# Optimization experiments

Hardware: AMD Instinct MI355X
Metric: run time of the kernel (lower is better)

The kernel has to match this reference:

```python
import jax, jax.numpy as jnp
import numpy as np

N_NODES = 100000
N_EDGES = 1000000
IN_F = 64
HID = 64
N_GRAPHS = 1000
HEADS = 4
NOTES = 128
NUM_MPNNS = 4
NUM_CONVS = 2
NUM_LINEARS = 3  # num_hidden_layers=2 -> 3 Linear layers in GIN MLP
EPS_BN = 1e-5


def setup_inputs() -> dict:
    key = jax.random.key(0)
    ks = jax.random.split(key, 16)
    s = 0.05
    x = jax.random.normal(ks[0], (N_NODES, IN_F), dtype=jnp.float32)
    edge_index = jax.random.randint(ks[1], (2, N_EDGES), 0, N_NODES)
    batch = jnp.sort(jax.random.randint(ks[2], (N_NODES,), 0, N_GRAPHS))
    dh = HID // HEADS
    return {
        'x': x,
        'edge_index': edge_index,
        'batch': batch,
        # feature BatchNorm affine params
        'fn_gamma': jnp.ones((IN_F,), jnp.float32),
        'fn_beta': jnp.zeros((IN_F,), jnp.float32),
        # input projection
        'proj_W': jax.random.normal(ks[3], (IN_F, HID), jnp.float32) * s,
        'proj_b': jnp.zeros((HID,), jnp.float32),
        # GIN MLPs: [num_mpnns, num_linears, HID, HID]
        'mlp_W': jax.random.normal(ks[4], (NUM_MPNNS, NUM_LINEARS, HID, HID), jnp.float32) * s,
        'mlp_b': jnp.zeros((NUM_MPNNS, NUM_LINEARS, HID), jnp.float32),
        # per-block conv BatchNorm affine params
        'norm_gamma': jnp.ones((NUM_MPNNS, HID), jnp.float32),
        'norm_beta': jnp.zeros((NUM_MPNNS, HID), jnp.float32),
        # attention readout (PMA-style): learned seed query per head
        'attn_seed': jax.random.normal(ks[5], (HEADS, dh), jnp.float32) * s,
        'attn_Wk': jax.random.normal(ks[6], (HID, HID), jnp.float32) * s,
        'attn_Wv': jax.random.normal(ks[7], (HID, HID), jnp.float32) * s,
        'attn_Wo': jax.random.normal(ks[8], (HID, HID), jnp.float32) * s,
        # notes predictor
        'pred_W': jax.random.normal(ks[9], (HID, NOTES), jnp.float32) * s,
        'pred_b': jnp.zeros((NOTES,), jnp.float32),
    }


def _batchnorm(z, gamma, beta):
    # training-mode BatchNorm1d over the node dimension (biased variance)
    mu = jnp.mean(z, axis=0)
    var = jnp.var(z, axis=0)
    return (z - mu) * jax.lax.rsqrt(var + EPS_BN) * gamma + beta


def reference(x, edge_index, batch, fn_gamma, fn_beta, proj_W, proj_b,
              mlp_W, mlp_b, norm_gamma, norm_beta,
              attn_seed, attn_Wk, attn_Wv, attn_Wo, pred_W, pred_b):
    src, dst = edge_index[0], edge_index[1]

    # feature norm + projection (dropout = identity at inference)
    h = _batchnorm(x, fn_gamma, fn_beta)
    h = jax.nn.relu(h @ proj_W + proj_b)
    residual = h

    # GINConv blocks: h' = MLP((1+eps)*h + sum_{j in N(i)} h_j), eps=0
    for m in range(NUM_MPNNS):
        for _ in range(NUM_CONVS):
            agg = h + jax.ops.segment_sum(h[src], dst, num_segments=N_NODES)
            z = agg
            for l in range(NUM_LINEARS):
                z = z @ mlp_W[m, l] + mlp_b[m, l]
                if l < NUM_LINEARS - 1:
                    z = jax.nn.relu(z)
            z = _batchnorm(z, norm_gamma[m], norm_beta[m])
            h = jax.nn.relu(z)
        h = h + residual
        residual = h

    # attention readout (PMA-style set attention pooling per graph)
    dh = HID // HEADS
    k = (h @ attn_Wk).reshape(N_NODES, HEADS, dh)
    v = (h @ attn_Wv).reshape(N_NODES, HEADS, dh)
    scores = jnp.einsum('nhd,hd->nh', k, attn_seed) / jnp.sqrt(jnp.float32(dh))
    smax = jax.ops.segment_max(scores, batch, num_segments=N_GRAPHS)  # [G,H]
    e = jnp.exp(scores - smax[batch])
    denom = jax.ops.segment_sum(e, batch, num_segments=N_GRAPHS)  # [G,H]
    attn = e / denom[batch]  # [N,H]
    pooled = jax.ops.segment_sum(attn[:, :, None] * v, batch, num_segments=N_GRAPHS)  # [G,H,dh]
    embed = pooled.reshape(N_GRAPHS, HID) @ attn_Wo  # [G, HID]

    logits = embed @ pred_W + pred_b
    return embed, logits
```

## Files before the change

kernel.cpp:

```cpp
#include <hip/hip_runtime.h>

typedef __attribute__((ext_vector_type(8))) short bf16x8;
typedef __attribute__((ext_vector_type(4))) float floatx4;

__device__ __forceinline__ unsigned short f2bf(float f)
{
    union { float f; unsigned int u; } v; v.f = f;
    unsigned int r = (v.u + 0x7fffu + ((v.u >> 16) & 1u)) >> 16;
    return (unsigned short)r;
}
__device__ __forceinline__ float bf2f(unsigned short b)
{
    union { unsigned int u; float f; } v; v.u = ((unsigned int)b) << 16;
    return v.f;
}

#define MFMA3(accv, ah, al, bh, bl)                                              \
    accv = __builtin_amdgcn_mfma_f32_16x16x32_bf16(ah, bh, accv, 0, 0, 0);       \
    accv = __builtin_amdgcn_mfma_f32_16x16x32_bf16(al, bh, accv, 0, 0, 0);       \
    accv = __builtin_amdgcn_mfma_f32_16x16x32_bf16(ah, bl, accv, 0, 0, 0);

#define BFRAG(P, n, kc, qd) (*(const bf16x8*)((P) + ((n) << 6) + (kc) * 32 + (qd) * 8))

__device__ __forceinline__ void pack_pair(const float* f, bf16x8& hi, bf16x8& lo)
{
#pragma unroll
    for (int j = 0; j < 8; ++j) {
        unsigned short hb = f2bf(f[j]);
        hi[j] = (short)hb;
        lo[j] = (short)f2bf(f[j] - bf2f(hb));
    }
}

__device__ __forceinline__ floatx4 gxform(uint2 raw, floatx4 sc4, floatx4 sh4)
{
    floatx4 v;
    v[0] = bf2f((unsigned short)(raw.x & 0xffffu));
    v[1] = bf2f((unsigned short)(raw.x >> 16));
    v[2] = bf2f((unsigned short)(raw.y & 0xffffu));
    v[3] = bf2f((unsigned short)(raw.y >> 16));
    floatx4 r;
#pragma unroll
    for (int j = 0; j < 4; ++j) r[j] = fmaxf(fmaf(v[j], sc4[j], sh4[j]), 0.f);
    return r;
}


__global__ void k_prep(const float* __restrict__ pW, const float* __restrict__ mlpW,
                       const float* __restrict__ Wv,
                       short* __restrict__ preH, short* __restrict__ preL)
{
    int mat = blockIdx.x;
    const float* Wg = (mat == 0) ? pW : ((mat <= 12) ? mlpW + (size_t)(mat - 1) * 4096 : Wv);
    int t = threadIdx.x;
    short* dh = preH + (size_t)mat * 4096;
    short* dl = preL + (size_t)mat * 4096;
#pragma unroll
    for (int i = 0; i < 16; ++i) {
        int idx = i * 256 + t;
        int k = idx >> 6, n = idx & 63;
        float w = Wg[idx];
        unsigned short hb = f2bf(w);
        dh[n * 64 + k] = (short)hb;
        dl[n * 64 + k] = (short)f2bf(w - bf2f(hb));
    }
}


__global__ void k_count(const int* __restrict__ dst, int* __restrict__ cnt, int E)
{
    for (int e = blockIdx.x * 256 + threadIdx.x; e < E; e += gridDim.x * 256)
        atomicAdd(&cnt[dst[e]], 1);
}

__global__ void k_scan1(const int* __restrict__ cnt, int* __restrict__ bsum, int n)
{
    __shared__ int red[256];
    int t = threadIdx.x;
    int i = blockIdx.x * 256 + t;
    red[t] = (i < n) ? cnt[i] : 0;
    __syncthreads();
    for (int off = 128; off; off >>= 1) {
        if (t < off) red[t] += red[t + off];
        __syncthreads();
    }
    if (t == 0) bsum[blockIdx.x] = red[0];
}

__global__ void k_scan2(const int* __restrict__ bsum, int* __restrict__ boff,
                        int nb, int* __restrict__ rowptrN)
{
    __shared__ int sc[512];
    int t = threadIdx.x;
    int v = (t < nb) ? bsum[t] : 0;
    sc[t] = v;
    __syncthreads();
    for (int off = 1; off < 512; off <<= 1) {
        int u = (t >= off) ? sc[t - off] : 0;
        __syncthreads();
        sc[t] += u;
        __syncthreads();
    }
    if (t < nb) boff[t] = sc[t] - v;
    if (t == nb - 1) *rowptrN = sc[t];
}

__global__ void k_scan3(int* __restrict__ cnt, const int* __restrict__ boff,
                        int* __restrict__ rowptr, int n)
{
    __shared__ int sc[256];
    int t = threadIdx.x;
    int i = blockIdx.x * 256 + t;
    int v = (i < n) ? cnt[i] : 0;
    sc[t] = v;
    __syncthreads();
    for (int off = 1; off < 256; off <<= 1) {
        int u = (t >= off) ? sc[t - off] : 0;
        __syncthreads();
        sc[t] += u;
        __syncthreads();
    }
    if (i < n) {
        rowptr[i] = boff[blockIdx.x] + sc[t] - v;
        cnt[i] = 0;
    }
}

__global__ void k_fill(const int* __restrict__ src, const int* __restrict__ dst,
                       const int* __restrict__ rowptr, int* __restrict__ cursor,
                       int* __restrict__ col, int E)
{
    for (int e = blockIdx.x * 256 + threadIdx.x; e < E; e += gridDim.x * 256) {
        int d = dst[e];
        int p = atomicAdd(&cursor[d], 1);
        col[rowptr[d] + p] = src[e];
    }
}


__global__ void k_xstats(const float* __restrict__ x, float* __restrict__ stats, int N)
{
    __shared__ float rs[256], rq[256];
    int t = threadIdx.x;
    int f = t & 63, rg = t >> 6;
    float s = 0.f, q = 0.f;
    for (int r = blockIdx.x * 4 + rg; r < N; r += gridDim.x * 4) {
        float v = x[(size_t)r * 64 + f];
        s += v; q += v * v;
    }
    rs[rg * 64 + f] = s; rq[rg * 64 + f] = q;
    __syncthreads();
    if (t < 64) {
        float ts = rs[t] + rs[64 + t] + rs[128 + t] + rs[192 + t];
        float tq = rq[t] + rq[64 + t] + rq[128 + t] + rq[192 + t];
        int rep = (blockIdx.x & 3) * 128;
        atomicAdd(&stats[rep + t], ts);
        atomicAdd(&stats[rep + 64 + t], tq);
    }
}

__device__ __forceinline__ void finalize_lds(const float* __restrict__ stats,
                                             const float* __restrict__ gamma,
                                             const float* __restrict__ beta,
                                             float* __restrict__ SS, int t, float invN)
{
    if (t < 64) {
        float su = stats[t] + stats[128 + t] + stats[256 + t] + stats[384 + t];
        float qu = stats[64 + t] + stats[192 + t] + stats[320 + t] + stats[448 + t];
        float mu = su * invN;
        float var = qu * invN - mu * mu;
        float sc = gamma[t] * rsqrtf(var + 1e-5f);
        SS[t] = sc;
        SS[64 + t] = beta[t] - mu * sc;
    }
}


__global__ void __launch_bounds__(256, 4)
k_proj(const float* __restrict__ x, const float* __restrict__ stats,
       const float* __restrict__ fn_g, const float* __restrict__ fn_b,
       const short* __restrict__ WH, const short* __restrict__ WL,
       const float* __restrict__ b,
       unsigned short* __restrict__ hbh, unsigned short* __restrict__ hbl,
       int N, float invN)
{
    __shared__ float ScSh[128];
    __shared__ float BiasSh[64];
    int t = threadIdx.x;
    int wave = t >> 6, lane = t & 63;
    int m = lane & 15, qd = lane >> 4;
    int base = blockIdx.x * 64;
    int nodeA = base + wave * 16 + m;

    finalize_lds(stats, fn_g, fn_b, ScSh, t, invN);
    if (t < 64) BiasSh[t] = b[t];
    __syncthreads();

    int rowc = min(nodeA, N - 1);
    bf16x8 ah[2], al[2];
#pragma unroll
    for (int kc = 0; kc < 2; ++kc) {
        floatx4 x0 = *(const floatx4*)(x + (size_t)rowc * 64 + kc * 32 + qd * 8);
        floatx4 x1 = *(const floatx4*)(x + (size_t)rowc * 64 + kc * 32 + qd * 8 + 4);
        float av[8];
#pragma unroll
        for (int j = 0; j < 8; ++j) {
            int k = kc * 32 + qd * 8 + j;
            float xv = (j < 4) ? x0[j] : x1[j - 4];
            av[j] = xv * ScSh[k] + ScSh[64 + k];
        }
        pack_pair(av, ah[kc], al[kc]);
    }

    floatx4 acc[4];
#pragma unroll
    for (int tt = 0; tt < 4; ++tt) {
        float bv = BiasSh[tt * 16 + m];
        acc[tt] = (floatx4){bv, bv, bv, bv};
    }
#pragma unroll
    for (int kc = 0; kc < 2; ++kc)
#pragma unroll
        for (int tt = 0; tt < 4; ++tt) {
            bf16x8 bh = BFRAG(WH, tt * 16 + m, kc, qd);
            bf16x8 bl = BFRAG(WL, tt * 16 + m, kc, qd);
            MFMA3(acc[tt], ah[kc], al[kc], bh, bl);
        }

#pragma unroll
    for (int tt = 0; tt < 4; ++tt)
#pragma unroll
        for (int r = 0; r < 4; ++r) {
            int node = base + wave * 16 + qd * 4 + r;
            if (node < N) {
                int col = tt * 16 + m;
                float v = fmaxf(acc[tt][r], 0.f);
                size_t off = (size_t)node * 64 + col;
                unsigned short ph = f2bf(v);
                hbh[off] = ph;
                hbl[off] = f2bf(v - bf2f(ph));
            }
        }
}


__global__ void __launch_bounds__(256, 8)
k_conv(const unsigned short* __restrict__ gsrc,
       const int* __restrict__ rowptr, const int* __restrict__ col,
       const short* __restrict__ WH, const short* __restrict__ WL,
       const float* __restrict__ b3,
       const float* __restrict__ pstats, const float* __restrict__ gamma,
       const float* __restrict__ beta,
       float* __restrict__ zout, unsigned short* __restrict__ zbout,
       float* __restrict__ stats, int N, int mode, float invN)
{
    __shared__ __align__(16) float Aint[64 * 68];
    __shared__ float BiasSh[192];
    __shared__ __align__(16) float SS[128];
    int t = threadIdx.x;
    int wave = t >> 6, lane = t & 63;
    int m = lane & 15, qd = lane >> 4;
    int base = blockIdx.x * 64;
    float* Aw = Aint + wave * 1088;

    if (t < 192) BiasSh[t] = b3[t];
    if (mode) {
        finalize_lds(pstats, gamma, beta, SS, t, invN);
    } else if (t < 128) {
        SS[t] = (t < 64) ? 1.f : 0.f;
    }
    __syncthreads();

    int g4 = lane >> 4;
    int fq = lane & 15;
    floatx4 sc4 = *(const floatx4*)(SS + 4 * fq);
    floatx4 sh4 = *(const floatx4*)(SS + 64 + 4 * fq);
    const unsigned short* gp = gsrc + fq * 4;

#pragma unroll 1
    for (int i = 0; i < 16; ++i) {
        int node = base + wave * 16 + i;
        floatx4 a4 = {0.f, 0.f, 0.f, 0.f};
        if (node < N) {
            {
                uint2 raw = *(const uint2*)(gp + (size_t)node * 64);
                floatx4 vv = gxform(raw, sc4, sh4);
                if (g4 == 0) a4 += vv;
            }
            int e0 = rowptr[node], e1 = rowptr[node + 1];
            int e = e0;
            for (; e + 8 <= e1; e += 8) {
                int s0 = col[e + g4], s1 = col[e + 4 + g4];
                uint2 r0 = *(const uint2*)(gp + (size_t)s0 * 64);
                uint2 r1 = *(const uint2*)(gp + (size_t)s1 * 64);
                a4 += gxform(r0, sc4, sh4);
                a4 += gxform(r1, sc4, sh4);
            }
            if (e + 4 <= e1) {
                int s0 = col[e + g4];
                uint2 r0 = *(const uint2*)(gp + (size_t)s0 * 64);
                a4 += gxform(r0, sc4, sh4);
                e += 4;
            }
            if (e < e1) {
                int ee = e + g4;
                int s0 = col[min(ee, e1 - 1)];
                uint2 r0 = *(const uint2*)(gp + (size_t)s0 * 64);
                floatx4 vv = gxform(r0, sc4, sh4);
                if (ee < e1) a4 += vv;
            }
#pragma unroll
            for (int j = 0; j < 4; ++j) {
                float v = a4[j];
                v += __shfl_xor(v, 16, 64);
                v += __shfl_xor(v, 32, 64);
                a4[j] = v;
            }
        }
        if (g4 == 0) *(floatx4*)(Aw + i * 68 + fq * 4) = a4;
    }
    __syncthreads();

    floatx4 acc[4];

#pragma unroll 1
    for (int l = 0; l < 3; ++l) {
        const short* LH = WH + l * 4096;
        const short* LL = WL + l * 4096;
#pragma unroll
        for (int tt = 0; tt < 4; ++tt) {
            float bv = BiasSh[l * 64 + tt * 16 + m];
            acc[tt] = (floatx4){bv, bv, bv, bv};
        }
#pragma unroll
        for (int kc = 0; kc < 2; ++kc) {
            floatx4 x0 = *(const floatx4*)(Aw + m * 68 + kc * 32 + qd * 8);
            floatx4 x1 = *(const floatx4*)(Aw + m * 68 + kc * 32 + qd * 8 + 4);
            float av[8];
#pragma unroll
            for (int j = 0; j < 8; ++j) av[j] = (j < 4) ? x0[j] : x1[j - 4];
            bf16x8 ah, al;
            pack_pair(av, ah, al);
#pragma unroll
            for (int tt = 0; tt < 4; ++tt) {
                bf16x8 bh = BFRAG(LH, tt * 16 + m, kc, qd);
                bf16x8 bl = BFRAG(LL, tt * 16 + m, kc, qd);
                MFMA3(acc[tt], ah, al, bh, bl);
            }
        }
        if (l < 2) {
            __syncthreads();
#pragma unroll
            for (int tt = 0; tt < 4; ++tt)
#pragma unroll
                for (int r = 0; r < 4; ++r)
                    Aw[(qd * 4 + r) * 68 + tt * 16 + m] = fmaxf(acc[tt][r], 0.f);
            __syncthreads();
        }
    }

#pragma unroll
    for (int tt = 0; tt < 4; ++tt)
#pragma unroll
        for (int r = 0; r < 4; ++r) {
            int node = base + wave * 16 + qd * 4 + r;
            if (node < N) {
                size_t off = (size_t)node * 64 + tt * 16 + m;
                if (mode) zout[off] = acc[tt][r];
                else      zbout[off] = f2bf(acc[tt][r]);
            }
        }

    __syncthreads();
    float* SW = Aint;
#pragma unroll
    for (int tt = 0; tt < 4; ++tt) {
        float s = 0.f, q = 0.f;
#pragma unroll
        for (int r = 0; r < 4; ++r) {
            int node = base + wave * 16 + qd * 4 + r;
            float v = (node < N) ? acc[tt][r] : 0.f;
            s += v; q += v * v;
        }
        SW[(tt * 16 + m) * 16 + wave * 4 + qd] = s;
        SW[2048 + (tt * 16 + m) * 16 + wave * 4 + qd] = q;
    }
    __syncthreads();
    if (t < 64) {
        float s = 0.f, q = 0.f;
#pragma unroll
        for (int i = 0; i < 16; ++i) { s += SW[t * 16 + i]; q += SW[2048 + t * 16 + i]; }
        int rep = (blockIdx.x & 3) * 128;
        atomicAdd(&stats[rep + t], s);
        atomicAdd(&stats[rep + 64 + t], q);
    }
}


__global__ void k_bnrelu(const float4* __restrict__ z4,
                         const float* __restrict__ stats, const float* __restrict__ gamma,
                         const float* __restrict__ beta,
                         ushort4* __restrict__ hbh4, ushort4* __restrict__ hbl4,
                         int total4, float invN)
{
    __shared__ float SS[128];
    int t = threadIdx.x;
    finalize_lds(stats, gamma, beta, SS, t, invN);
    __syncthreads();
    for (int idx = blockIdx.x * 256 + t; idx < total4; idx += gridDim.x * 256) {
        int c = (idx & 15) << 2;
        float4 v = z4[idx];
        ushort4 rh = hbh4[idx];
        ushort4 rl = hbl4[idx];
        v.x = fmaxf(v.x * SS[c + 0] + SS[64 + c + 0], 0.f) + (bf2f(rh.x) + bf2f(rl.x));
        v.y = fmaxf(v.y * SS[c + 1] + SS[64 + c + 1], 0.f) + (bf2f(rh.y) + bf2f(rl.y));
        v.z = fmaxf(v.z * SS[c + 2] + SS[64 + c + 2], 0.f) + (bf2f(rh.z) + bf2f(rl.z));
        v.w = fmaxf(v.w * SS[c + 3] + SS[64 + c + 3], 0.f) + (bf2f(rh.w) + bf2f(rl.w));
        ushort4 ph, pl;
        ph.x = f2bf(v.x); ph.y = f2bf(v.y); ph.z = f2bf(v.z); ph.w = f2bf(v.w);
        pl.x = f2bf(v.x - bf2f(ph.x));
        pl.y = f2bf(v.y - bf2f(ph.y));
        pl.z = f2bf(v.z - bf2f(ph.z));
        pl.w = f2bf(v.w - bf2f(ph.w));
        hbh4[idx] = ph;
        hbl4[idx] = pl;
    }
}


__global__ void __launch_bounds__(256, 4)
k_bnvs(const float* __restrict__ z,
       const unsigned short* __restrict__ hbh, const unsigned short* __restrict__ hbl,
       const float* __restrict__ stats, const float* __restrict__ gamma,
       const float* __restrict__ beta,
       const short* __restrict__ WH, const short* __restrict__ WL,
       const float* __restrict__ Wk, const float* __restrict__ seed,
       float* __restrict__ v, float* __restrict__ scores, int N, float invN)
{
    __shared__ float ScSh[128];
    __shared__ short Sh[16 * 72], Sl[16 * 72];
    int t = threadIdx.x;
    int wave = t >> 6, lane = t & 63;
    int m = lane & 15, qd = lane >> 4;
    int base = blockIdx.x * 64;
    int nodeA = base + wave * 16 + m;

    finalize_lds(stats, gamma, beta, ScSh, t, invN);
    {
        int k = t >> 2, n = t & 3;
        float s = 0.f;
#pragma unroll
        for (int d = 0; d < 16; ++d) s += Wk[k * 64 + n * 16 + d] * seed[n * 16 + d];
        s *= 0.25f;
        unsigned short hb = f2bf(s);
        Sh[n * 72 + k] = (short)hb;
        Sl[n * 72 + k] = (short)f2bf(s - bf2f(hb));
        unsigned int* Z1 = (unsigned int*)(Sh + 4 * 72);
        unsigned int* Z2 = (unsigned int*)(Sl + 4 * 72);
        for (int idx2 = t; idx2 < 432; idx2 += 256) { Z1[idx2] = 0; Z2[idx2] = 0; }
    }
    __syncthreads();

    int rowc = min(nodeA, N - 1);
    bf16x8 ah[2], al[2];
#pragma unroll
    for (int kc = 0; kc < 2; ++kc) {
        floatx4 z0 = *(const floatx4*)(z + (size_t)rowc * 64 + kc * 32 + qd * 8);
        floatx4 z1 = *(const floatx4*)(z + (size_t)rowc * 64 + kc * 32 + qd * 8 + 4);
        bf16x8 rh = *(const bf16x8*)(hbh + (size_t)rowc * 64 + kc * 32 + qd * 8);
        bf16x8 rl = *(const bf16x8*)(hbl + (size_t)rowc * 64 + kc * 32 + qd * 8);
        float av[8];
#pragma unroll
        for (int j = 0; j < 8; ++j) {
            int k = kc * 32 + qd * 8 + j;
            float zv = (j < 4) ? z0[j] : z1[j - 4];
            float rv = bf2f((unsigned short)rh[j]) + bf2f((unsigned short)rl[j]);
            av[j] = fmaxf(zv * ScSh[k] + ScSh[64 + k], 0.f) + rv;
        }
        pack_pair(av, ah[kc], al[kc]);
    }

    floatx4 acc[5] = {};
#pragma unroll
    for (int kc = 0; kc < 2; ++kc) {
#pragma unroll
        for (int tt = 0; tt < 4; ++tt) {
            bf16x8 bh = BFRAG(WH, tt * 16 + m, kc, qd);
            bf16x8 bl = BFRAG(WL, tt * 16 + m, kc, qd);
            MFMA3(acc[tt], ah[kc], al[kc], bh, bl);
        }
        bf16x8 sh = *(const bf16x8*)(Sh + m * 72 + kc * 32 + qd * 8);
        bf16x8 sl = *(const bf16x8*)(Sl + m * 72 + kc * 32 + qd * 8);
        MFMA3(acc[4], ah[kc], al[kc], sh, sl);
    }

#pragma unroll
    for (int tt = 0; tt < 4; ++tt)
#pragma unroll
        for (int r = 0; r < 4; ++r) {
            int node = base + wave * 16 + qd * 4 + r;
            if (node < N)
                v[(size_t)node * 64 + tt * 16 + m] = acc[tt][r];
        }
    if (m < 4) {
#pragma unroll
        for (int r = 0; r < 4; ++r) {
            int node = base + wave * 16 + qd * 4 + r;
            if (node < N) scores[(size_t)node * 4 + m] = acc[4][r];
        }
    }
}


__global__ void k_tail(const float4* __restrict__ scores4, const float* __restrict__ v,
                       const int* __restrict__ batch,
                       const float* __restrict__ Wo, const float* __restrict__ predW,
                       const float* __restrict__ predb,
                       float* __restrict__ emb, float* __restrict__ logits, int N)
{
    int g = blockIdx.x;
    int t = threadIdx.x;
    __shared__ int sb[2];
    __shared__ float4 rmax[256];
    __shared__ float racc[256];
    __shared__ float resum[16];
    __shared__ float pooledSh[64];
    __shared__ float embSh[64];
    if (t < 2) {
        int target = g + t;
        int lo = 0, hi = N;
        while (lo < hi) {
            int mid = (lo + hi) >> 1;
            if (batch[mid] < target) lo = mid + 1; else hi = mid;
        }
        sb[t] = lo;
    }
    __syncthreads();
    int s = sb[0], e = sb[1];
    if (s >= e) {
        if (t < 64) pooledSh[t] = 0.f;
    } else {
        float4 m = make_float4(-1e30f, -1e30f, -1e30f, -1e30f);
        for (int i = s + t; i < e; i += 256) {
            float4 sc = scores4[i];
            m.x = fmaxf(m.x, sc.x); m.y = fmaxf(m.y, sc.y);
            m.z = fmaxf(m.z, sc.z); m.w = fmaxf(m.w, sc.w);
        }
        rmax[t] = m;
        __syncthreads();
        for (int off = 128; off; off >>= 1) {
            if (t < off) {
                float4 a = rmax[t], b = rmax[t + off];
                a.x = fmaxf(a.x, b.x); a.y = fmaxf(a.y, b.y);
                a.z = fmaxf(a.z, b.z); a.w = fmaxf(a.w, b.w);
                rmax[t] = a;
            }
            __syncthreads();
        }
        float4 smax = rmax[0];
        int rg = t >> 6, f = t & 63, hh = f >> 4;
        float mx = (hh == 0) ? smax.x : ((hh == 1) ? smax.y : ((hh == 2) ? smax.z : smax.w));
        float acc = 0.f, es = 0.f;
        for (int i = s + rg; i < e; i += 4) {
            float4 sc = scores4[i];
            float scl = (hh == 0) ? sc.x : ((hh == 1) ? sc.y : ((hh == 2) ? sc.z : sc.w));
            float ev = __expf(scl - mx);
            acc += ev * v[(size_t)i * 64 + f];
            if ((f & 15) == 0) es += ev;
        }
        racc[rg * 64 + f] = acc;
        if ((f & 15) == 0) resum[rg * 4 + hh] = es;
        __syncthreads();
        if (t < 64) {
            float tot = racc[t] + racc[64 + t] + racc[128 + t] + racc[192 + t];
            int h2 = t >> 4;
            float den = resum[h2] + resum[4 + h2] + resum[8 + h2] + resum[12 + h2];
            pooledSh[t] = tot / den;
        }
    }
    __syncthreads();

    if (t < 64) {
        float s2 = 0.f;
#pragma unroll 4
        for (int k = 0; k < 64; ++k) s2 = fmaf(pooledSh[k], Wo[k * 64 + t], s2);
        embSh[t] = s2;
        emb[(size_t)g * 64 + t] = s2;
    }
    __syncthreads();

    if (t < 128) {
        float s2 = predb[t];
#pragma unroll 4
        for (int k = 0; k < 64; ++k) s2 = fmaf(embSh[k], predW[k * 128 + t], s2);
        logits[(size_t)g * 128 + t] = s2;
    }
}


extern "C" void kernel_launch(void* const* d_in, const int* in_sizes, int n_in,
                              void* d_out, int out_size, void* d_ws, size_t ws_size,
                              hipStream_t stream)
{
    const float* x     = (const float*)d_in[0];
    const int*   eidx  = (const int*)d_in[1];
    const int*   batch = (const int*)d_in[2];
    const float* fn_g  = (const float*)d_in[3];
    const float* fn_b  = (const float*)d_in[4];
    const float* pW    = (const float*)d_in[5];
    const float* pb    = (const float*)d_in[6];
    const float* mlpW  = (const float*)d_in[7];
    const float* mlpb  = (const float*)d_in[8];
    const float* ngm   = (const float*)d_in[9];
    const float* nbt   = (const float*)d_in[10];
    const float* seed  = (const float*)d_in[11];
    const float* Wk    = (const float*)d_in[12];
    const float* Wv    = (const float*)d_in[13];
    const float* Wo    = (const float*)d_in[14];
    const float* predW = (const float*)d_in[15];
    const float* predb = (const float*)d_in[16];

    const int N = 100000, E = 1000000, G = 1000;
    const int* srcv = eidx;
    const int* dstv = eidx + E;

    char* w = (char*)d_ws;
    auto alloc = [&](size_t bytes) {
        char* p = w;
        w += (bytes + 255) & ~(size_t)255;
        return p;
    };
    const size_t NPAD = 100032;
    float*          z    = (float*)alloc(NPAD * 64 * 4);
    unsigned short* hbh  = (unsigned short*)alloc(NPAD * 64 * 2);
    unsigned short* hbl  = (unsigned short*)alloc(NPAD * 64 * 2);
    unsigned short* zb   = (unsigned short*)alloc(NPAD * 64 * 2);
    short* preH = (short*)alloc(14 * 4096 * 2);
    short* preL = (short*)alloc(14 * 4096 * 2);
    int*   rowptr = (int*)alloc((size_t)(N + 1) * 4);
    int*   cnt    = (int*)alloc((size_t)N * 4);
    int*   col    = (int*)alloc((size_t)E * 4);
    int*   bsum   = (int*)alloc(512 * 4);
    int*   boff   = (int*)alloc(512 * 4);
    float* stats  = (float*)alloc(9 * 512 * 4);
    float* scores = (float*)alloc(NPAD * 4 * 4);

    float* emb    = (float*)d_out;
    float* logits = (float*)d_out + G * 64;

    const int NB = (N + 63) / 64;
    const int NBS = (N + 255) / 256;
    const float invN = 1.f / (float)N;

    hipMemsetAsync(cnt, 0, (size_t)N * 4, stream);
    hipMemsetAsync(stats, 0, 9 * 512 * 4, stream);
    k_prep<<<14, 256, 0, stream>>>(pW, mlpW, Wv, preH, preL);
    k_count<<<1024, 256, 0, stream>>>(dstv, cnt, E);
    k_scan1<<<NBS, 256, 0, stream>>>(cnt, bsum, N);
    k_scan2<<<1, 512, 0, stream>>>(bsum, boff, NBS, rowptr + N);
    k_scan3<<<NBS, 256, 0, stream>>>(cnt, boff, rowptr, N);
    k_fill<<<1024, 256, 0, stream>>>(srcv, dstv, rowptr, cnt, col, E);

    k_xstats<<<512, 256, 0, stream>>>(x, stats, N);
    k_proj<<<NB, 256, 0, stream>>>(x, stats, fn_g, fn_b, preH, preL, pb, hbh, hbl, N, invN);

    for (int m = 0; m < 4; ++m) {
        int mat = 1 + m * 3;
        const short* WH = preH + (size_t)mat * 4096;
        const short* WL = preL + (size_t)mat * 4096;
        const float* b3 = mlpb + (size_t)m * 3 * 64;
        float* st0 = stats + (size_t)(1 + m * 2) * 512;
        float* st1 = stats + (size_t)(2 + m * 2) * 512;

        k_conv<<<NB, 256, 0, stream>>>(hbh, rowptr, col, WH, WL, b3,
                                       nullptr, nullptr, nullptr,
                                       nullptr, zb, st0, N, 0, invN);
        k_conv<<<NB, 256, 0, stream>>>(zb, rowptr, col, WH, WL, b3,
                                       st0, ngm + m * 64, nbt + m * 64,
                                       z, nullptr, st1, N, 1, invN);
        if (m < 3)
            k_bnrelu<<<2048, 256, 0, stream>>>(
                (const float4*)z, st1, ngm + m * 64, nbt + m * 64,
                (ushort4*)hbh, (ushort4*)hbl, N * 16, invN);
    }

    float* vbuf = z;
    k_bnvs<<<NB, 256, 0, stream>>>(z, hbh, hbl, stats + 8 * 512, ngm + 192, nbt + 192,
                                   preH + 13 * 4096, preL + 13 * 4096,
                                   Wk, seed, vbuf, scores, N, invN);
    k_tail<<<G, 256, 0, stream>>>((const float4*)scores, vbuf, batch,
                                  Wo, predW, predb, emb, logits, N);
}
```

Baseline: 955.6 us.

## Merge setup kernels: fold memsets into prep, co-launch count/xstats and fill/proj

```diff
diff --git a/kernel.cpp b/kernel.cpp
--- a/kernel.cpp
+++ b/kernel.cpp
@@ -48,103 +48,46 @@
 
 __global__ void k_prep(const float* __restrict__ pW, const float* __restrict__ mlpW,
                        const float* __restrict__ Wv,
-                       short* __restrict__ preH, short* __restrict__ preL)
-{
-    int mat = blockIdx.x;
-    const float* Wg = (mat == 0) ? pW : ((mat <= 12) ? mlpW + (size_t)(mat - 1) * 4096 : Wv);
-    int t = threadIdx.x;
-    short* dh = preH + (size_t)mat * 4096;
-    short* dl = preL + (size_t)mat * 4096;
-#pragma unroll
-    for (int i = 0; i < 16; ++i) {
-        int idx = i * 256 + t;
-        int k = idx >> 6, n = idx & 63;
-        float w = Wg[idx];
-        unsigned short hb = f2bf(w);
-        dh[n * 64 + k] = (short)hb;
-        dl[n * 64 + k] = (short)f2bf(w - bf2f(hb));
-    }
-}
-
-
-__global__ void k_count(const int* __restrict__ dst, int* __restrict__ cnt, int E)
-{
-    for (int e = blockIdx.x * 256 + threadIdx.x; e < E; e += gridDim.x * 256)
-        atomicAdd(&cnt[dst[e]], 1);
-}
-
-__global__ void k_scan1(const int* __restrict__ cnt, int* __restrict__ bsum, int n)
-{
-    __shared__ int red[256];
-    int t = threadIdx.x;
-    int i = blockIdx.x * 256 + t;
-    red[t] = (i < n) ? cnt[i] : 0;
-    __syncthreads();
-    for (int off = 128; off; off >>= 1) {
-        if (t < off) red[t] += red[t + off];
-        __syncthreads();
-    }
-    if (t == 0) bsum[blockIdx.x] = red[0];
-}
-
-__global__ void k_scan2(const int* __restrict__ bsum, int* __restrict__ boff,
-                        int nb, int* __restrict__ rowptrN)
-{
-    __shared__ int sc[512];
-    int t = threadIdx.x;
-    int v = (t < nb) ? bsum[t] : 0;
-    sc[t] = v;
-    __syncthreads();
-    for (int off = 1; off < 512; off <<= 1) {
-        int u = (t >= off) ? sc[t - off] : 0;
-        __syncthreads();
-        sc[t] += u;
-        __syncthreads();
-    }
-    if (t < nb) boff[t] = sc[t] - v;
-    if (t == nb - 1) *rowptrN = sc[t];
-}
-
-__global__ void k_scan3(int* __restrict__ cnt, const int* __restrict__ boff,
-                        int* __restrict__ rowptr, int n)
-{
-    __shared__ int sc[256];
-    int t = threadIdx.x;
-    int i = blockIdx.x * 256 + t;
-    int v = (i < n) ? cnt[i] : 0;
-    sc[t] = v;
-    __syncthreads();
-    for (int off = 1; off < 256; off <<= 1) {
-        int u = (t >= off) ? sc[t - off] : 0;
-        __syncthreads();
-        sc[t] += u;
-        __syncthreads();
-    }
-    if (i < n) {
-        rowptr[i] = boff[blockIdx.x] + sc[t] - v;
-        cnt[i] = 0;
-    }
-}
-
-__global__ void k_fill(const int* __restrict__ src, const int* __restrict__ dst,
-                       const int* __restrict__ rowptr, int* __restrict__ cursor,
-                       int* __restrict__ col, int E)
-{
-    for (int e = blockIdx.x * 256 + threadIdx.x; e < E; e += gridDim.x * 256) {
-        int d = dst[e];
-        int p = atomicAdd(&cursor[d], 1);
-        col[rowptr[d] + p] = src[e];
-    }
-}
-
-
-__global__ void k_xstats(const float* __restrict__ x, float* __restrict__ stats, int N)
-{
+                       short* __restrict__ preH, short* __restrict__ preL,
+                       int* __restrict__ cnt, float* __restrict__ stats, int N)
+{
+    int b = blockIdx.x, t = threadIdx.x;
+    int total = N + 9 * 512;
+    for (int i = b * 256 + t; i < total; i += gridDim.x * 256) {
+        if (i < N) cnt[i] = 0;
+        else stats[i - N] = 0.f;
+    }
+    if (b < 14) {
+        const float* Wg = (b == 0) ? pW : ((b <= 12) ? mlpW + (size_t)(b - 1) * 4096 : Wv);
+        short* dh = preH + (size_t)b * 4096;
+        short* dl = preL + (size_t)b * 4096;
+#pragma unroll
+        for (int i = 0; i < 16; ++i) {
+            int idx = i * 256 + t;
+            int k = idx >> 6, n = idx & 63;
+            float w = Wg[idx];
+            unsigned short hb = f2bf(w);
+            dh[n * 64 + k] = (short)hb;
+            dl[n * 64 + k] = (short)f2bf(w - bf2f(hb));
+        }
+    }
+}
+
+
+__global__ void k_cx(const float* __restrict__ x, float* __restrict__ stats,
+                     const int* __restrict__ dst, int* __restrict__ cnt, int N, int E)
+{
+    if ((int)blockIdx.x >= 512) {
+        int b = blockIdx.x - 512;
+        for (int e = b * 256 + threadIdx.x; e < E; e += 512 * 256)
+            atomicAdd(&cnt[dst[e]], 1);
+        return;
+    }
     __shared__ float rs[256], rq[256];
     int t = threadIdx.x;
     int f = t & 63, rg = t >> 6;
     float s = 0.f, q = 0.f;
-    for (int r = blockIdx.x * 4 + rg; r < N; r += gridDim.x * 4) {
+    for (int r = blockIdx.x * 4 + rg; r < N; r += 512 * 4) {
         float v = x[(size_t)r * 64 + f];
         s += v; q += v * v;
     }
@@ -156,6 +99,60 @@
         int rep = (blockIdx.x & 3) * 128;
         atomicAdd(&stats[rep + t], ts);
         atomicAdd(&stats[rep + 64 + t], tq);
+    }
+}
+
+
+__global__ void k_scan1(const int* __restrict__ cnt, int* __restrict__ bsum, int n)
+{
+    __shared__ int red[256];
+    int t = threadIdx.x;
+    int i = blockIdx.x * 256 + t;
+    red[t] = (i < n) ? cnt[i] : 0;
+    __syncthreads();
+    for (int off = 128; off; off >>= 1) {
+        if (t < off) red[t] += red[t + off];
+        __syncthreads();
+    }
+    if (t == 0) bsum[blockIdx.x] = red[0];
+}
+
+__global__ void k_scan2(const int* __restrict__ bsum, int* __restrict__ boff,
+                        int nb, int* __restrict__ rowptrN)
+{
+    __shared__ int sc[512];
+    int t = threadIdx.x;
+    int v = (t < nb) ? bsum[t] : 0;
+    sc[t] = v;
+    __syncthreads();
+    for (int off = 1; off < 512; off <<= 1) {
+        int u = (t >= off) ? sc[t - off] : 0;
+        __syncthreads();
+        sc[t] += u;
+        __syncthreads();
+    }
+    if (t < nb) boff[t] = sc[t] - v;
+    if (t == nb - 1) *rowptrN = sc[t];
+}
+
+__global__ void k_scan3(int* __restrict__ cnt, const int* __restrict__ boff,
+                        int* __restrict__ rowptr, int n)
+{
+    __shared__ int sc[256];
+    int t = threadIdx.x;
+    int i = blockIdx.x * 256 + t;
+    int v = (i < n) ? cnt[i] : 0;
+    sc[t] = v;
+    __syncthreads();
+    for (int off = 1; off < 256; off <<= 1) {
+        int u = (t >= off) ? sc[t - off] : 0;
+        __syncthreads();
+        sc[t] += u;
+        __syncthreads();
+    }
+    if (i < n) {
+        rowptr[i] = boff[blockIdx.x] + sc[t] - v;
+        cnt[i] = 0;
     }
 }
 
@@ -177,13 +174,25 @@
 
 
 __global__ void __launch_bounds__(256, 4)
-k_proj(const float* __restrict__ x, const float* __restrict__ stats,
-       const float* __restrict__ fn_g, const float* __restrict__ fn_b,
-       const short* __restrict__ WH, const short* __restrict__ WL,
-       const float* __restrict__ b,
-       unsigned short* __restrict__ hbh, unsigned short* __restrict__ hbl,
-       int N, float invN)
-{
+k_fp(const float* __restrict__ x, const float* __restrict__ stats,
+     const float* __restrict__ fn_g, const float* __restrict__ fn_b,
+     const short* __restrict__ WH, const short* __restrict__ WL,
+     const float* __restrict__ b,
+     unsigned short* __restrict__ hbh, unsigned short* __restrict__ hbl,
+     const int* __restrict__ src, const int* __restrict__ dst,
+     const int* __restrict__ rowptr, int* __restrict__ cursor, int* __restrict__ col,
+     int N, int E, int NB, float invN)
+{
+    if ((int)blockIdx.x >= NB) {
+        int bb = blockIdx.x - NB;
+        for (int e = bb * 256 + threadIdx.x; e < E; e += 512 * 256) {
+            int d = dst[e];
+            int p = atomicAdd(&cursor[d], 1);
+            col[rowptr[d] + p] = src[e];
+        }
+        return;
+    }
+
     __shared__ float ScSh[128];
     __shared__ float BiasSh[64];
     int t = threadIdx.x;
@@ -233,9 +242,9 @@
         for (int r = 0; r < 4; ++r) {
             int node = base + wave * 16 + qd * 4 + r;
             if (node < N) {
-                int col = tt * 16 + m;
+                int c_ = tt * 16 + m;
                 float v = fmaxf(acc[tt][r], 0.f);
-                size_t off = (size_t)node * 64 + col;
+                size_t off = (size_t)node * 64 + c_;
                 unsigned short ph = f2bf(v);
                 hbh[off] = ph;
                 hbl[off] = f2bf(v - bf2f(ph));
@@ -652,17 +661,15 @@
     const int NBS = (N + 255) / 256;
     const float invN = 1.f / (float)N;
 
-    hipMemsetAsync(cnt, 0, (size_t)N * 4, stream);
-    hipMemsetAsync(stats, 0, 9 * 512 * 4, stream);
-    k_prep<<<14, 256, 0, stream>>>(pW, mlpW, Wv, preH, preL);
-    k_count<<<1024, 256, 0, stream>>>(dstv, cnt, E);
+    k_prep<<<128, 256, 0, stream>>>(pW, mlpW, Wv, preH, preL, cnt, stats, N);
+    k_cx<<<1024, 256, 0, stream>>>(x, stats, dstv, cnt, N, E);
     k_scan1<<<NBS, 256, 0, stream>>>(cnt, bsum, N);
     k_scan2<<<1, 512, 0, stream>>>(bsum, boff, NBS, rowptr + N);
     k_scan3<<<NBS, 256, 0, stream>>>(cnt, boff, rowptr, N);
-    k_fill<<<1024, 256, 0, stream>>>(srcv, dstv, rowptr, cnt, col, E);
-
-    k_xstats<<<512, 256, 0, stream>>>(x, stats, N);
-    k_proj<<<NB, 256, 0, stream>>>(x, stats, fn_g, fn_b, preH, preL, pb, hbh, hbl, N, invN);
+
+    k_fp<<<NB + 512, 256, 0, stream>>>(x, stats, fn_g, fn_b, preH, preL, pb,
+                                       hbh, hbl, srcv, dstv, rowptr, cnt, col,
+                                       N, E, NB, invN);
 
     for (int m = 0; m < 4; ++m) {
         int mat = 1 + m * 3;
```

New measurement: 915.2 us. 4.2% less time.
